# Kernel optimization log

Hardware: AMD Instinct MI355X
Metric: run time of the kernel (lower is better)

Reference implementation:

```python
import jax, jax.numpy as jnp
import numpy as np

BLANK = 0
BEAM = 5


def setup_inputs() -> dict:
    key = jax.random.key(0)
    ks = jax.random.split(key, 8)
    B, T, H, V = 8, 128, 1024, 4096
    s = lambda k, sh, sc: jax.random.normal(k, sh, dtype=jnp.float32) * sc
    return {
        "tn_output": s(ks[0], (B, T, H), 1.0),
        "E": s(ks[1], (V, H), 0.02),
        "W_ih": s(ks[2], (4 * H, H), 0.02),
        "W_hh": s(ks[3], (4 * H, H), 0.02),
        "b_lstm": jnp.zeros((4 * H,), jnp.float32),
        "W_tn": s(ks[4], (H, H), 0.02),
        "W_pn": s(ks[5], (H, H), 0.02),
        "b_joint": jnp.zeros((H,), jnp.float32),
        "W_out": s(ks[6], (H, V), 0.02),
        "b_out": jnp.zeros((V,), jnp.float32),
    }


def _beam_search(tn_output, E, W_ih, W_hh, b_lstm, W_tn, W_pn, b_joint, W_out, b_out):
    # Batched RNN-T beam search (one expansion per frame, all B*K hyps batched).
    B, T, H = tn_output.shape
    V = E.shape[0]
    K = BEAM
    NEG = jnp.float32(-1e9)

    tn_proj = jnp.einsum('bth,hd->btd', tn_output, W_tn)  # [B,T,H] precomputed

    tokens0 = jnp.full((B, K), BLANK, jnp.int32)          # last emitted token
    h0 = jnp.zeros((B, K, H), tn_output.dtype)
    c0 = jnp.zeros((B, K, H), tn_output.dtype)
    scores0 = jnp.full((B, K), NEG).at[:, 0].set(0.0)     # only beam 0 alive
    preds0 = jnp.zeros((B, K, T), jnp.int32)
    lens0 = jnp.zeros((B, K), jnp.int32)

    def step(carry, tn_t):  # tn_t: [B,H] (projected TN output at frame t)
        tokens, h, c, scores, preds, lens = carry
        # --- prediction network (LSTM cell) over all B*K hyps at once ---
        emb = E[tokens]                                   # [B,K,H]
        gates = emb @ W_ih.T + h @ W_hh.T + b_lstm        # [B,K,4H]
        i_g, f_g, g_g, o_g = jnp.split(gates, 4, axis=-1)
        c_new = jax.nn.sigmoid(f_g) * c + jax.nn.sigmoid(i_g) * jnp.tanh(g_g)
        h_new = jax.nn.sigmoid(o_g) * jnp.tanh(c_new)     # [B,K,H]
        # --- joint network ---
        joint = jnp.tanh(tn_t[:, None, :] + h_new @ W_pn + b_joint)
        logp = jax.nn.log_softmax(joint @ W_out + b_out, axis=-1)  # [B,K,V]
        # --- beam expand + prune ---
        cand = (scores[:, :, None] + logp).reshape(B, K * V)
        top_s, top_i = jax.lax.top_k(cand, K)             # [B,K]
        parent = top_i // V
        tok = (top_i % V).astype(jnp.int32)
        is_blank = tok == BLANK

        g2 = lambda x: jnp.take_along_axis(x, parent, axis=1)
        g3 = lambda x: jnp.take_along_axis(x, parent[:, :, None], axis=1)
        # blank keeps the parent's pre-step decoder state; non-blank advances it
        h_next = jnp.where(is_blank[:, :, None], g3(h), g3(h_new))
        c_next = jnp.where(is_blank[:, :, None], g3(c), g3(c_new))
        tokens_next = jnp.where(is_blank, g2(tokens), tok)
        lens_p = g2(lens)
        preds_p = g3(preds.reshape(B, K, -1)).reshape(B, K, preds.shape[-1])
        pos = (jnp.arange(preds.shape[-1])[None, None, :] == lens_p[:, :, None]) & (~is_blank)[:, :, None]
        preds_next = jnp.where(pos, tok[:, :, None], preds_p)
        lens_next = lens_p + (~is_blank).astype(jnp.int32)
        return (tokens_next, h_next, c_next, top_s, preds_next, lens_next), None

    carry, _ = jax.lax.scan(step, (tokens0, h0, c0, scores0, preds0, lens0),
                            jnp.swapaxes(tn_proj, 0, 1))
    _, _, _, scores, preds, lens = carry
    # original normalizes by len(prediction) which includes the leading blank -> lens+1
    norm = scores / (lens.astype(scores.dtype) + 1.0)
    return preds, lens, norm


def reference(tn_output, E, W_ih, W_hh, b_lstm, W_tn, W_pn, b_joint, W_out, b_out):
    preds, lens, norm = _beam_search(tn_output, E, W_ih, W_hh, b_lstm,
                                     W_tn, W_pn, b_joint, W_out, b_out)
    best = jnp.argmax(norm, axis=1)                       # [B]
    best_preds = jnp.take_along_axis(preds, best[:, None, None], axis=1)[:, 0]  # [B,T]
    best_lens = jnp.take_along_axis(lens, best[:, None], axis=1)[:, 0]          # [B]
    mean_score = jnp.exp(jnp.max(norm, axis=1)).mean()
    return best_preds, best_lens, mean_score, norm
```

## Files before the change

### kernel.cpp

```cpp
#include <hip/hip_runtime.h>
#include <math.h>

#define HH 1024
#define VV 4096
#define TSTEPS 128
#define NB 256
#define NT 512

typedef float  floatx4 __attribute__((ext_vector_type(4)));
typedef int    intx4   __attribute__((ext_vector_type(4)));


__device__ __forceinline__ float sigf(float x) { return 1.0f / (1.0f + expf(-x)); }

__device__ __forceinline__ float rowsum16(float x) {
  x += __int_as_float(__builtin_amdgcn_update_dpp(0, __float_as_int(x), 0x111, 0xf, 0xf, true));
  x += __int_as_float(__builtin_amdgcn_update_dpp(0, __float_as_int(x), 0x112, 0xf, 0xf, true));
  x += __int_as_float(__builtin_amdgcn_update_dpp(0, __float_as_int(x), 0x114, 0xf, 0xf, true));
  x += __int_as_float(__builtin_amdgcn_update_dpp(0, __float_as_int(x), 0x118, 0xf, 0xf, true));
  return x;
}

__device__ __forceinline__ void ins5(float* bv, int* bi, float v, int i) {
#pragma unroll
  for (int j = 0; j < 5; ++j) {
    if (v > bv[j] || (v == bv[j] && i < bi[j])) {
#pragma unroll
      for (int s = 4; s > j; --s) { bv[s] = bv[s - 1]; bi[s] = bi[s - 1]; }
      bv[j] = v; bi[j] = i;
      break;
    }
  }
}


__device__ __forceinline__ float ldcc(const float* p) {
  float v;
  asm volatile("global_load_dword %0, %1, off sc0 sc1\n\ts_waitcnt vmcnt(0)"
               : "=&v"(v) : "v"(p) : "memory");
  return v;
}
__device__ __forceinline__ int ldcci(const int* p) {
  int v;
  asm volatile("global_load_dword %0, %1, off sc0 sc1\n\ts_waitcnt vmcnt(0)"
               : "=&v"(v) : "v"(p) : "memory");
  return v;
}
__device__ __forceinline__ floatx4 ldcc4(const float* p) {
  floatx4 v;
  asm volatile("global_load_dwordx4 %0, %1, off sc0 sc1\n\ts_waitcnt vmcnt(0)"
               : "=&v"(v) : "v"(p) : "memory");
  return v;
}
__device__ __forceinline__ void stcc(float* p, float v) {
  asm volatile("global_store_dword %0, %1, off sc0 sc1" :: "v"(p), "v"(v) : "memory");
}
__device__ __forceinline__ void stcci(int* p, int v) {
  asm volatile("global_store_dword %0, %1, off sc0 sc1" :: "v"(p), "v"(v) : "memory");
}
__device__ __forceinline__ void stcc4(float* p, floatx4 v) {
  asm volatile("global_store_dwordx4 %0, %1, off sc0 sc1" :: "v"(p), "v"(v) : "memory");
}
__device__ __forceinline__ void stcc4i(int* p, intx4 v) {
  asm volatile("global_store_dwordx4 %0, %1, off sc0 sc1" :: "v"(p), "v"(v) : "memory");
}

__device__ __forceinline__ void ldwt(floatx4& v, const float* p) {
  asm volatile("global_load_dwordx4 %0, %1, off\n\ts_waitcnt vmcnt(0)"
               : "=&v"(v) : "v"(p));
}

__device__ __forceinline__ void ldcc4x5(const float* p0, const float* p1, const float* p2,
                                        const float* p3, const float* p4,
                                        floatx4& v0, floatx4& v1, floatx4& v2,
                                        floatx4& v3, floatx4& v4) {
  asm volatile(
      "global_load_dwordx4 %0, %5, off sc0 sc1\n\t"
      "global_load_dwordx4 %1, %6, off sc0 sc1\n\t"
      "global_load_dwordx4 %2, %7, off sc0 sc1\n\t"
      "global_load_dwordx4 %3, %8, off sc0 sc1\n\t"
      "global_load_dwordx4 %4, %9, off sc0 sc1\n\t"
      "s_waitcnt vmcnt(0)"
      : "=&v"(v0), "=&v"(v1), "=&v"(v2), "=&v"(v3), "=&v"(v4)
      : "v"(p0), "v"(p1), "v"(p2), "v"(p3), "v"(p4)
      : "memory");
}

__device__ __forceinline__ void ldcc_top5(const float* pv, const int* pi,
                                          float tv[5], int ti[5]) {
  floatx4 a; float a1; intx4 b; int b1;
  asm volatile(
      "global_load_dwordx4 %0, %4, off sc0 sc1\n\t"
      "global_load_dword   %1, %5, off sc0 sc1\n\t"
      "global_load_dwordx4 %2, %6, off sc0 sc1\n\t"
      "global_load_dword   %3, %7, off sc0 sc1\n\t"
      "s_waitcnt vmcnt(0)"
      : "=&v"(a), "=&v"(a1), "=&v"(b), "=&v"(b1)
      : "v"(pv), "v"(pv + 4), "v"(pi), "v"(pi + 4)
      : "memory");
  tv[0] = a.x; tv[1] = a.y; tv[2] = a.z; tv[3] = a.w; tv[4] = a1;
  ti[0] = b.x; ti[1] = b.y; ti[2] = b.z; ti[3] = b.w; ti[4] = b1;
}

__device__ __forceinline__ void ldcc_state(const float* ps, const int* pl, const int* pt,
                                           const int* pp, const int* pb,
                                           float& sc, int& ln, int& tk, int& pr, int& bl) {
  asm volatile(
      "global_load_dword %0, %5, off sc0 sc1\n\t"
      "global_load_dword %1, %6, off sc0 sc1\n\t"
      "global_load_dword %2, %7, off sc0 sc1\n\t"
      "global_load_dword %3, %8, off sc0 sc1\n\t"
      "global_load_dword %4, %9, off sc0 sc1\n\t"
      "s_waitcnt vmcnt(0)"
      : "=&v"(sc), "=&v"(ln), "=&v"(tk), "=&v"(pr), "=&v"(bl)
      : "v"(ps), "v"(pl), "v"(pt), "v"(pp), "v"(pb)
      : "memory");
}


__global__ __launch_bounds__(256) void k_transp(const float* __restrict__ in,
                                                float* __restrict__ out, int R, int C) {
  __shared__ float tile[32][33];
  int c0 = blockIdx.x * 32, r0 = blockIdx.y * 32;
  int tx = threadIdx.x & 31, ty = threadIdx.x >> 5;
#pragma unroll
  for (int i = 0; i < 32; i += 8) tile[ty + i][tx] = in[(long)(r0 + ty + i) * C + c0 + tx];
  __syncthreads();
#pragma unroll
  for (int i = 0; i < 32; i += 8) out[(long)(c0 + ty + i) * R + r0 + tx] = tile[tx][ty + i];
}

__global__ __launch_bounds__(256) void k_tnproj(const float* __restrict__ A,
                                                const float* __restrict__ B,
                                                float* __restrict__ C) {
  __shared__ float As[64][20];
  __shared__ float Bs[16][68];
  int tid = threadIdx.x, blk = blockIdx.x;
  int bx = blk & 15, by = blk >> 4;
  int tx = tid & 15, ty = tid >> 4;
  float acc[4][4];
#pragma unroll
  for (int i = 0; i < 4; i++)
#pragma unroll
    for (int j = 0; j < 4; j++) acc[i][j] = 0.f;
  for (int k0 = 0; k0 < 1024; k0 += 16) {
    {
      int row = tid >> 2, q = tid & 3;
      float4 v = *(const float4*)&A[(long)(by * 64 + row) * 1024 + k0 + q * 4];
      As[row][q * 4] = v.x; As[row][q * 4 + 1] = v.y; As[row][q * 4 + 2] = v.z; As[row][q * 4 + 3] = v.w;
    }
    {
      int row = tid >> 4, q = tid & 15;
      float4 v = *(const float4*)&B[(long)(k0 + row) * 1024 + bx * 64 + q * 4];
      *(float4*)&Bs[row][q * 4] = v;
    }
    __syncthreads();
#pragma unroll
    for (int kk = 0; kk < 16; kk++) {
      float a0 = As[ty * 4][kk], a1 = As[ty * 4 + 1][kk], a2 = As[ty * 4 + 2][kk], a3 = As[ty * 4 + 3][kk];
      float4 b4 = *(const float4*)&Bs[kk][tx * 4];
      acc[0][0] += a0 * b4.x; acc[0][1] += a0 * b4.y; acc[0][2] += a0 * b4.z; acc[0][3] += a0 * b4.w;
      acc[1][0] += a1 * b4.x; acc[1][1] += a1 * b4.y; acc[1][2] += a1 * b4.z; acc[1][3] += a1 * b4.w;
      acc[2][0] += a2 * b4.x; acc[2][1] += a2 * b4.y; acc[2][2] += a2 * b4.z; acc[2][3] += a2 * b4.w;
      acc[3][0] += a3 * b4.x; acc[3][1] += a3 * b4.y; acc[3][2] += a3 * b4.z; acc[3][3] += a3 * b4.w;
    }
    __syncthreads();
  }
#pragma unroll
  for (int i = 0; i < 4; i++) {
    float4 v = make_float4(acc[i][0], acc[i][1], acc[i][2], acc[i][3]);
    *(float4*)&C[(long)(by * 64 + ty * 4 + i) * 1024 + bx * 64 + tx * 4] = v;
  }
}


__global__ __launch_bounds__(NT, 1) void k_beam(
    const float* __restrict__ E, const float* __restrict__ Wih,
    const float* __restrict__ Whh, const float* __restrict__ b_lstm,
    const float* __restrict__ tn_proj, const float* __restrict__ WpnT,
    const float* __restrict__ b_joint, const float* __restrict__ WoutT,
    const float* __restrict__ b_out,
    float* __restrict__ h_pre0, float* __restrict__ h_pre1,
    float* __restrict__ c_pre0, float* __restrict__ c_pre1,
    float* __restrict__ h_new0, float* __restrict__ h_new1,
    float* __restrict__ c_new0, float* __restrict__ c_new1,
    float* __restrict__ joint, float* __restrict__ expsum_part,
    float* __restrict__ top5v, int* __restrict__ top5i,
    int* __restrict__ preds0, int* __restrict__ preds1,
    float* __restrict__ gscores, int* __restrict__ glens,
    int* __restrict__ gtokens, int* __restrict__ gpar, int* __restrict__ gblank,
    unsigned int* bar, float* __restrict__ out) {
  int tid = threadIdx.x, blk = blockIdx.x;
  int wav = tid >> 6, lane = tid & 63;

  __shared__ float xs[10240];
  __shared__ float part[640];
  __shared__ float s_scores[40], s_scls[5];
  __shared__ int s_tokens[40], s_lens[40], s_par[40], s_blank[40];
  __shared__ float s_csel[160];
  __shared__ float wtv[40];
  __shared__ int wti[40];
  __shared__ int s_best[8];
  __shared__ float s_maxn[8];
  float4* xs4 = (float4*)xs;

  floatx4 wihr[2][4], whhr[2][4], wpnr[4], woutr[2][4];
#pragma unroll
  for (int rr = 0; rr < 2; ++rr) {
    int gr = wav * 2 + rr;
    int jg = blk * 4 + (gr >> 2), g = gr & 3;
#pragma unroll
    for (int c = 0; c < 4; ++c) {
      ldwt(wihr[rr][c], &Wih[(long)(g * HH + jg) * HH + c * 256 + lane * 4]);
      ldwt(whhr[rr][c], &Whh[(long)(g * HH + jg) * HH + c * 256 + lane * 4]);
    }
  }
  {
    int d = blk * 4 + (wav >> 1);
#pragma unroll
    for (int c = 0; c < 4; ++c)
      ldwt(wpnr[c], &WpnT[(long)d * HH + c * 256 + lane * 4]);
  }
#pragma unroll
  for (int r = 0; r < 2; ++r) {
    int v = blk * 16 + wav * 2 + r;
#pragma unroll
    for (int c = 0; c < 4; ++c)
      ldwt(woutr[r][c], &WoutT[(long)v * HH + c * 256 + lane * 4]);
  }

  if (tid < 40) {
    s_scores[tid] = ((tid % 5) == 0) ? 0.f : -1e9f;
    s_tokens[tid] = 0; s_lens[tid] = 0; s_par[tid] = tid; s_blank[tid] = 1;
  }
  __syncthreads();

  unsigned int round = 0;
  auto gsync = [&]() {
    asm volatile("s_waitcnt vmcnt(0)" ::: "memory");
    __syncthreads();
    if (tid == 0)
      __hip_atomic_fetch_add(&bar[(blk & 15) * 16], 1u, __ATOMIC_RELAXED, __HIP_MEMORY_SCOPE_AGENT);
    ++round;
    if (tid < 16) {
      unsigned int tgt = round * 16u;
      while (__hip_atomic_load(&bar[tid * 16], __ATOMIC_RELAXED, __HIP_MEMORY_SCOPE_AGENT) < tgt)
        __builtin_amdgcn_s_sleep(2);
    }
    __syncthreads();
  };

  auto preds_update = [&](int u) {
    const int* pip = ((u - 1) & 1) ? preds1 : preds0;
    int* pop = (u & 1) ? preds1 : preds0;
    int m0 = blk * 10;
    for (int cell = tid; cell < 1280; cell += NT) {
      int j = cell >> 7, pos = cell & 127, gj = m0 + j;
      int isb = s_blank[gj];
      int plen = s_lens[gj] - (isb ? 0 : 1);
      int v = ldcci(&pip[s_par[gj] * 128 + pos]);
      if (!isb && pos == plen) v = s_tokens[gj];
      stcci(&pop[gj * 128 + pos], v);
    }
  };

  for (int t = 0; t < TSTEPS; ++t) {
    const float* h_pre_in = (t & 1) ? h_pre1 : h_pre0;
    const float* h_new_in = (t & 1) ? h_new1 : h_new0;
    const float* c_pre_in = (t & 1) ? c_pre1 : c_pre0;
    const float* c_new_in = (t & 1) ? c_new1 : c_new0;
    float* h_pre_o = (t & 1) ? h_pre0 : h_pre1;
    float* h_new_o = (t & 1) ? h_new0 : h_new1;
    float* c_pre_o = (t & 1) ? c_pre0 : c_pre1;
    float* c_new_o = (t & 1) ? c_new0 : c_new1;

    if (t > 0) {
      if (tid < 40) {
        float sc; int ln, tk, pr, bl;
        ldcc_state(&gscores[tid], &glens[tid], &gtokens[tid], &gpar[tid], &gblank[tid],
                   sc, ln, tk, pr, bl);
        s_scores[tid] = sc; s_lens[tid] = ln; s_tokens[tid] = tk;
        s_par[tid] = pr; s_blank[tid] = bl;
      }
      __syncthreads();
      if (tid < 160) {
        int mg = tid >> 2, j = tid & 3;
        const float* cb = s_blank[mg] ? c_pre_in : c_new_in;
        s_csel[tid] = ldcc(&cb[(long)s_par[mg] * HH + blk * 4 + j]);
      }
      if (blk < 4) preds_update(t);
    }

    {
      int mat = tid >> 8, k4f = (tid & 255) * 4;
      for (int cc = 0; cc < 8; ++cc) {
        int ch = (blk + cc) & 7;
        int mbase = ch * 5;
        if (mat == 0) {
#pragma unroll
          for (int i = 0; i < 5; ++i)
            xs4[i * 512 + tid] = *(const float4*)&E[(long)s_tokens[mbase + i] * HH + k4f];
        } else if (t == 0) {
          floatx4 z = {0.f, 0.f, 0.f, 0.f};
#pragma unroll
          for (int i = 0; i < 5; ++i) {
            *(floatx4*)(xs4 + i * 512 + tid) = z;
            if (blk == ch) stcc4(&h_pre_o[(long)(mbase + i) * HH + k4f], z);
          }
        } else {
          const float* p[5];
#pragma unroll
          for (int i = 0; i < 5; ++i) {
            int mg = mbase + i;
            const float* hb = s_blank[mg] ? h_pre_in : h_new_in;
            p[i] = &hb[(long)s_par[mg] * HH + k4f];
          }
          floatx4 v0, v1, v2, v3, v4;
          ldcc4x5(p[0], p[1], p[2], p[3], p[4], v0, v1, v2, v3, v4);
          *(floatx4*)(xs4 + 0 * 512 + tid) = v0;
          *(floatx4*)(xs4 + 1 * 512 + tid) = v1;
          *(floatx4*)(xs4 + 2 * 512 + tid) = v2;
          *(floatx4*)(xs4 + 3 * 512 + tid) = v3;
          *(floatx4*)(xs4 + 4 * 512 + tid) = v4;
          if (blk == ch) {
            stcc4(&h_pre_o[(long)(mbase + 0) * HH + k4f], v0);
            stcc4(&h_pre_o[(long)(mbase + 1) * HH + k4f], v1);
            stcc4(&h_pre_o[(long)(mbase + 2) * HH + k4f], v2);
            stcc4(&h_pre_o[(long)(mbase + 3) * HH + k4f], v3);
            stcc4(&h_pre_o[(long)(mbase + 4) * HH + k4f], v4);
          }
        }
        __syncthreads();
        float acc[5][2];
#pragma unroll
        for (int m = 0; m < 5; ++m) { acc[m][0] = 0.f; acc[m][1] = 0.f; }
#pragma unroll
        for (int m = 0; m < 5; ++m) {
#pragma unroll
          for (int c = 0; c < 4; ++c) {
            float4 x = xs4[m * 512 + c * 64 + lane];
#pragma unroll
            for (int rr = 0; rr < 2; ++rr) {
              floatx4 ww = wihr[rr][c];
              acc[m][rr] += x.x * ww.x; acc[m][rr] += x.y * ww.y;
              acc[m][rr] += x.z * ww.z; acc[m][rr] += x.w * ww.w;
            }
          }
#pragma unroll
          for (int c = 0; c < 4; ++c) {
            float4 x = xs4[m * 512 + 256 + c * 64 + lane];
#pragma unroll
            for (int rr = 0; rr < 2; ++rr) {
              floatx4 ww = whhr[rr][c];
              acc[m][rr] += x.x * ww.x; acc[m][rr] += x.y * ww.y;
              acc[m][rr] += x.z * ww.z; acc[m][rr] += x.w * ww.w;
            }
          }
        }
#pragma unroll
        for (int m = 0; m < 5; ++m) {
          acc[m][0] = rowsum16(acc[m][0]);
          acc[m][1] = rowsum16(acc[m][1]);
        }
        if ((lane & 15) == 15) {
          int grp = lane >> 4;
#pragma unroll
          for (int m = 0; m < 5; ++m) {
            part[(wav * 4 + grp) * 10 + m * 2] = acc[m][0];
            part[(wav * 4 + grp) * 10 + m * 2 + 1] = acc[m][1];
          }
        }
        __syncthreads();
        if (tid < 20) {
          int mloc = tid >> 2, j = tid & 3;
          int mg = mbase + mloc, jglob = blk * 4 + j;
          float gi = 0.f, gf = 0.f, gg = 0.f, go = 0.f;
#pragma unroll
          for (int r = 0; r < 4; ++r) {
            gi += part[((j * 2) * 4 + r) * 10 + mloc * 2];
            gf += part[((j * 2) * 4 + r) * 10 + mloc * 2 + 1];
            gg += part[((j * 2 + 1) * 4 + r) * 10 + mloc * 2];
            go += part[((j * 2 + 1) * 4 + r) * 10 + mloc * 2 + 1];
          }
          gi += b_lstm[jglob]; gf += b_lstm[HH + jglob];
          gg += b_lstm[2 * HH + jglob]; go += b_lstm[3 * HH + jglob];
          float csel = (t == 0) ? 0.f : s_csel[mg * 4 + j];
          float cn = sigf(gf) * csel + sigf(gi) * tanhf(gg);
          float hn = sigf(go) * tanhf(cn);
          long o = (long)mg * HH + jglob;
          stcc(&h_new_o[o], hn); stcc(&c_new_o[o], cn); stcc(&c_pre_o[o], csel);
        }
      }
    }
    gsync();

    {
      int mrow = tid >> 8, k4f = (tid & 255) * 4;
      for (int cc = 0; cc < 4; ++cc) {
        int ch = (blk + cc) & 3;
        int mbase = ch * 10;
        floatx4 v0, v1, v2, v3, v4;
        ldcc4x5(&h_new_o[(long)(mbase + mrow + 0) * HH + k4f],
                &h_new_o[(long)(mbase + mrow + 2) * HH + k4f],
                &h_new_o[(long)(mbase + mrow + 4) * HH + k4f],
                &h_new_o[(long)(mbase + mrow + 6) * HH + k4f],
                &h_new_o[(long)(mbase + mrow + 8) * HH + k4f],
                v0, v1, v2, v3, v4);
        *(floatx4*)(xs4 + 0 * 512 + tid) = v0;
        *(floatx4*)(xs4 + 1 * 512 + tid) = v1;
        *(floatx4*)(xs4 + 2 * 512 + tid) = v2;
        *(floatx4*)(xs4 + 3 * 512 + tid) = v3;
        *(floatx4*)(xs4 + 4 * 512 + tid) = v4;
        __syncthreads();
        float accj[5];
#pragma unroll
        for (int m = 0; m < 5; ++m) accj[m] = 0.f;
        int mh = (wav & 1) * 5;
#pragma unroll
        for (int m = 0; m < 5; ++m) {
#pragma unroll
          for (int c = 0; c < 4; ++c) {
            float4 x = xs4[(mh + m) * 256 + c * 64 + lane];
            floatx4 ww = wpnr[c];
            accj[m] += x.x * ww.x; accj[m] += x.y * ww.y;
            accj[m] += x.z * ww.z; accj[m] += x.w * ww.w;
          }
        }
#pragma unroll
        for (int m = 0; m < 5; ++m) accj[m] = rowsum16(accj[m]);
        if ((lane & 15) == 15) {
          int grp = lane >> 4;
#pragma unroll
          for (int m = 0; m < 5; ++m) part[(wav * 4 + grp) * 5 + m] = accj[m];
        }
        __syncthreads();
        if (tid < 40) {
          int mloc = tid >> 2, d = tid & 3;
          int wv = d * 2 + (mloc >= 5 ? 1 : 0), m5 = mloc % 5;
          float s = 0.f;
#pragma unroll
          for (int r = 0; r < 4; ++r) s += part[(wv * 4 + r) * 5 + m5];
          int mg = mbase + mloc, dglob = blk * 4 + d, b = mg / 5;
          stcc(&joint[(long)mg * HH + dglob],
               tanhf(s + tn_proj[((long)b * TSTEPS + t) * HH + dglob] + b_joint[dglob]));
        }
      }
    }
    gsync();

    {
      int mrow = tid >> 8, k4f = (tid & 255) * 4;
      for (int cc = 0; cc < 4; ++cc) {
        int ch = (blk + cc) & 3;
        int mbase = ch * 10;
        floatx4 v0, v1, v2, v3, v4;
        ldcc4x5(&joint[(long)(mbase + mrow + 0) * HH + k4f],
                &joint[(long)(mbase + mrow + 2) * HH + k4f],
                &joint[(long)(mbase + mrow + 4) * HH + k4f],
                &joint[(long)(mbase + mrow + 6) * HH + k4f],
                &joint[(long)(mbase + mrow + 8) * HH + k4f],
                v0, v1, v2, v3, v4);
        *(floatx4*)(xs4 + 0 * 512 + tid) = v0;
        *(floatx4*)(xs4 + 1 * 512 + tid) = v1;
        *(floatx4*)(xs4 + 2 * 512 + tid) = v2;
        *(floatx4*)(xs4 + 3 * 512 + tid) = v3;
        *(floatx4*)(xs4 + 4 * 512 + tid) = v4;
        __syncthreads();
        float accl[10][2];
#pragma unroll
        for (int m = 0; m < 10; ++m) { accl[m][0] = 0.f; accl[m][1] = 0.f; }
#pragma unroll
        for (int m = 0; m < 10; ++m)
#pragma unroll
          for (int c = 0; c < 4; ++c) {
            float4 x = xs4[m * 256 + c * 64 + lane];
#pragma unroll
            for (int r = 0; r < 2; ++r) {
              floatx4 ww = woutr[r][c];
              accl[m][r] += x.x * ww.x; accl[m][r] += x.y * ww.y;
              accl[m][r] += x.z * ww.z; accl[m][r] += x.w * ww.w;
            }
          }
#pragma unroll
        for (int m = 0; m < 10; ++m) {
          accl[m][0] = rowsum16(accl[m][0]);
          accl[m][1] = rowsum16(accl[m][1]);
        }
        if ((lane & 15) == 15) {
          int grp = lane >> 4;
#pragma unroll
          for (int m = 0; m < 10; ++m) {
            part[(wav * 4 + grp) * 20 + m * 2] = accl[m][0];
            part[(wav * 4 + grp) * 20 + m * 2 + 1] = accl[m][1];
          }
        }
        __syncthreads();
        if (tid < 160) {
          int mloc = tid >> 4, vloc = tid & 15;
          int wv = vloc >> 1, rowr = vloc & 1;
          float s = 0.f;
#pragma unroll
          for (int r = 0; r < 4; ++r) s += part[(wv * 4 + r) * 20 + mloc * 2 + rowr];
          int v = blk * 16 + vloc, mg = mbase + mloc;
          float lg = s + b_out[v];
          float e = rowsum16(expf(lg));
          if ((tid & 15) == 15) stcc(&expsum_part[mg * 256 + blk], e);
          float cv = lg; int ci = (mg % 5) * 4096 + v;
          float tv[5]; int ti5[5];
#pragma unroll
          for (int r5 = 0; r5 < 5; ++r5) {
            float mv = cv; int mi = ci;
#pragma unroll
            for (int off2 = 1; off2 < 16; off2 <<= 1) {
              float ov = __shfl_xor(mv, off2, 16);
              int oi = __shfl_xor(mi, off2, 16);
              if (ov > mv || (ov == mv && oi < mi)) { mv = ov; mi = oi; }
            }
            if (cv == mv && ci == mi) cv = -3.0e38f;
            tv[r5] = mv; ti5[r5] = mi;
          }
          if ((tid & 15) == 0) {
            int toff = (mg * 256 + blk) * 8;
            floatx4 tvv = {tv[0], tv[1], tv[2], tv[3]};
            intx4 tiv = {ti5[0], ti5[1], ti5[2], ti5[3]};
            stcc4(&top5v[toff], tvv); stcc(&top5v[toff + 4], tv[4]);
            stcc4i(&top5i[toff], tiv); stcci(&top5i[toff + 4], ti5[4]);
          }
        }
      }
    }
    gsync();

    if (blk < 8) {
      int b = blk;
      if (wav < 5) {
        int kp = wav;
        const float* ep = &expsum_part[(b * 5 + kp) * 256];
        floatx4 e4 = ldcc4(&ep[lane * 4]);
        float tl = ((e4.x + e4.y) + e4.z) + e4.w;
        part[kp * 64 + lane] = tl;
        if (lane == 0) {
          float ssum = 0.f;
          for (int i = 0; i < 64; ++i) ssum += part[kp * 64 + i];
          s_scls[kp] = s_scores[b * 5 + kp] - logf(ssum);
        }
      }
      __syncthreads();
      float bv[5]; int bi5[5];
#pragma unroll
      for (int q = 0; q < 5; ++q) { bv[q] = -3.0e38f; bi5[q] = 0x7fffffff; }
      for (int e = wav * 160 + lane; e < wav * 160 + 160; e += 64) {
        int kp = e >> 8, blkc = e & 255;
        float base = s_scls[kp];
        int off = ((b * 5 + kp) * 256 + blkc) * 8;
        float tv[5]; int ti5[5];
        ldcc_top5(&top5v[off], &top5i[off], tv, ti5);
#pragma unroll
        for (int q = 0; q < 5; ++q) ins5(bv, bi5, tv[q] + base, ti5[q]);
      }
      float myv = 0.f; int myi = 0;
#pragma unroll
      for (int r = 0; r < 5; ++r) {
        float mv = bv[0]; int mi = bi5[0];
#pragma unroll
        for (int off2 = 1; off2 < 64; off2 <<= 1) {
          float ov = __shfl_xor(mv, off2, 64);
          int oi = __shfl_xor(mi, off2, 64);
          if (ov > mv || (ov == mv && oi < mi)) { mv = ov; mi = oi; }
        }
        if (bv[0] == mv && bi5[0] == mi) {
          bv[0] = bv[1]; bi5[0] = bi5[1]; bv[1] = bv[2]; bi5[1] = bi5[2];
          bv[2] = bv[3]; bi5[2] = bi5[3]; bv[3] = bv[4]; bi5[3] = bi5[4];
          bv[4] = -3.0e38f; bi5[4] = 0x7fffffff;
        }
        if (lane == r) { myv = mv; myi = mi; }
      }
      if (lane < 5) { wtv[wav * 5 + lane] = myv; wti[wav * 5 + lane] = myi; }
      __syncthreads();
      if (wav == 0) {
        float cv = (lane < 40) ? wtv[lane] : -3.0e38f;
        int ci = (lane < 40) ? wti[lane] : 0x7fffffff;
#pragma unroll
        for (int r = 0; r < 5; ++r) {
          float mv = cv; int mi = ci;
#pragma unroll
          for (int off2 = 1; off2 < 64; off2 <<= 1) {
            float ov = __shfl_xor(mv, off2, 64);
            int oi = __shfl_xor(mi, off2, 64);
            if (ov > mv || (ov == mv && oi < mi)) { mv = ov; mi = oi; }
          }
          if (cv == mv && ci == mi) cv = -3.0e38f;
          if (lane == r) { myv = mv; myi = mi; }
        }
        if (lane < 5) {
          int kp = myi >> 12, tok = myi & 4095;
          int isb = (tok == 0) ? 1 : 0;
          int pg = b * 5 + kp, slot = b * 5 + lane;
          stcc(&gscores[slot], myv); stcci(&gpar[slot], pg); stcci(&gblank[slot], isb);
          stcci(&gtokens[slot], isb ? s_tokens[pg] : tok);
          stcci(&glens[slot], s_lens[pg] + (isb ? 0 : 1));
        }
      }
    }
    gsync();
  }

  if (tid < 40) {
    float sc; int ln, tk, pr, bl;
    ldcc_state(&gscores[tid], &glens[tid], &gtokens[tid], &gpar[tid], &gblank[tid],
               sc, ln, tk, pr, bl);
    s_scores[tid] = sc; s_lens[tid] = ln; s_tokens[tid] = tk;
    s_par[tid] = pr; s_blank[tid] = bl;
  }
  __syncthreads();
  if (blk < 4) preds_update(TSTEPS);
  gsync();

  if (blk == 0) {
    if (tid < 40) out[1033 + tid] = s_scores[tid] / (float)(s_lens[tid] + 1);
    if (tid < 8) {
      float bvn = -3.0e38f; int bk = 0;
      for (int k = 0; k < 5; ++k) {
        float n = s_scores[tid * 5 + k] / (float)(s_lens[tid * 5 + k] + 1);
        if (n > bvn) { bvn = n; bk = k; }
      }
      s_best[tid] = bk; s_maxn[tid] = bvn;
      out[1024 + tid] = (float)s_lens[tid * 5 + bk];
    }
    __syncthreads();
    if (tid == 0) {
      float s = 0.f;
      for (int b = 0; b < 8; ++b) s += expf(s_maxn[b]);
      out[1032] = s / 8.f;
    }
    for (int cI = tid; cI < 1024; cI += NT) {
      int b = cI >> 7, pos = cI & 127;
      out[cI] = (float)ldcci(&preds0[(b * 5 + s_best[b]) * 128 + pos]);
    }
  }
}


extern "C" void kernel_launch(void* const* d_in, const int* in_sizes, int n_in,
                              void* d_out, int out_size, void* d_ws, size_t ws_size,
                              hipStream_t stream) {
  const float* tn   = (const float*)d_in[0];
  const float* E    = (const float*)d_in[1];
  const float* Wih  = (const float*)d_in[2];
  const float* Whh  = (const float*)d_in[3];
  const float* bl   = (const float*)d_in[4];
  const float* Wtn  = (const float*)d_in[5];
  const float* Wpn  = (const float*)d_in[6];
  const float* bj   = (const float*)d_in[7];
  const float* Wout = (const float*)d_in[8];
  const float* bo   = (const float*)d_in[9];
  float* out = (float*)d_out;

  unsigned int* bar = (unsigned int*)d_ws;
  float* w = (float*)d_ws + 256;
  size_t off = 0;
  float* tn_proj = w + off; off += 1048576;
  float* WpnT    = w + off; off += 1048576;
  float* WoutT   = w + off; off += 4194304;
  float* joint   = w + off; off += 40960;
  float* expsum  = w + off; off += 10240;
  float* top5v   = w + off; off += 81920;
  float* h_pre0  = w + off; off += 40960;
  float* h_pre1  = w + off; off += 40960;
  float* c_pre0  = w + off; off += 40960;
  float* c_pre1  = w + off; off += 40960;
  float* h_new0  = w + off; off += 40960;
  float* h_new1  = w + off; off += 40960;
  float* c_new0  = w + off; off += 40960;
  float* c_new1  = w + off; off += 40960;
  float* gscores = w + off; off += 40;
  int* ib = (int*)(w + off);
  int* top5i   = ib; ib += 81920;
  int* preds0  = ib; ib += 5120;
  int* preds1  = ib; ib += 5120;
  int* glens   = ib; ib += 40;
  int* gtokens = ib; ib += 40;
  int* gpar    = ib; ib += 40;
  int* gblank  = ib; ib += 40;
  if (ws_size < (size_t)(256 + off + 92320) * 4) return;

  hipMemsetAsync(bar, 0, 1024, stream);
  hipMemsetAsync(preds0, 0, 5120 * sizeof(int), stream);
  k_transp<<<dim3(32, 32), 256, 0, stream>>>(Wpn, WpnT, 1024, 1024);
  k_transp<<<dim3(128, 32), 256, 0, stream>>>(Wout, WoutT, 1024, 4096);
  k_tnproj<<<256, 256, 0, stream>>>(tn, Wtn, tn_proj);

  void* args[] = { (void*)&E, (void*)&Wih, (void*)&Whh, (void*)&bl,
                   (void*)&tn_proj, (void*)&WpnT, (void*)&bj, (void*)&WoutT, (void*)&bo,
                   (void*)&h_pre0, (void*)&h_pre1, (void*)&c_pre0, (void*)&c_pre1,
                   (void*)&h_new0, (void*)&h_new1, (void*)&c_new0, (void*)&c_new1,
                   (void*)&joint, (void*)&expsum, (void*)&top5v, (void*)&top5i,
                   (void*)&preds0, (void*)&preds1, (void*)&gscores, (void*)&glens,
                   (void*)&gtokens, (void*)&gpar, (void*)&gblank,
                   (void*)&bar, (void*)&out };
  hipLaunchCooperativeKernel((void*)k_beam, dim3(NB), dim3(NT), args, 0, stream);
}
```

Before: 12.54 ms.

## Triple-buffer activation loads via async global-to-LDS with prefetch in each phase

Replaces the synchronous register-staged loads of embeddings, hidden states, and joint activations with global_load_lds direct-to-LDS transfers into a three-slot LDS ring. Each phase prefetches up to three chunks ahead and uses counted vmcnt waits, so memory latency overlaps with the dot-product compute of earlier chunks. The preds copy is also unrolled so that all of its loads are issued together before a single wait. This triples the LDS footprint, which may reduce occupancy. It also relies on hand-tuned waitcnt counts and cache-coherence bits for data written by other blocks in the persistent kernel.

```diff
diff --git a/kernel.cpp b/kernel.cpp
--- a/kernel.cpp
+++ b/kernel.cpp
@@ -9,6 +9,10 @@
 
 typedef float  floatx4 __attribute__((ext_vector_type(4)));
 typedef int    intx4   __attribute__((ext_vector_type(4)));
+
+#define GLL(gp, lp, aux) __builtin_amdgcn_global_load_lds( \
+    (const __attribute__((address_space(1))) unsigned int*)(gp), \
+    (__attribute__((address_space(3))) unsigned int*)(lp), 16, 0, aux)
 
 
 __device__ __forceinline__ float sigf(float x) { return 1.0f / (1.0f + expf(-x)); }
@@ -68,22 +72,6 @@
 __device__ __forceinline__ void ldwt(floatx4& v, const float* p) {
   asm volatile("global_load_dwordx4 %0, %1, off\n\ts_waitcnt vmcnt(0)"
                : "=&v"(v) : "v"(p));
-}
-
-__device__ __forceinline__ void ldcc4x5(const float* p0, const float* p1, const float* p2,
-                                        const float* p3, const float* p4,
-                                        floatx4& v0, floatx4& v1, floatx4& v2,
-                                        floatx4& v3, floatx4& v4) {
-  asm volatile(
-      "global_load_dwordx4 %0, %5, off sc0 sc1\n\t"
-      "global_load_dwordx4 %1, %6, off sc0 sc1\n\t"
-      "global_load_dwordx4 %2, %7, off sc0 sc1\n\t"
-      "global_load_dwordx4 %3, %8, off sc0 sc1\n\t"
-      "global_load_dwordx4 %4, %9, off sc0 sc1\n\t"
-      "s_waitcnt vmcnt(0)"
-      : "=&v"(v0), "=&v"(v1), "=&v"(v2), "=&v"(v3), "=&v"(v4)
-      : "v"(p0), "v"(p1), "v"(p2), "v"(p3), "v"(p4)
-      : "memory");
 }
 
 __device__ __forceinline__ void ldcc_top5(const float* pv, const int* pi,
@@ -193,7 +181,7 @@
   int tid = threadIdx.x, blk = blockIdx.x;
   int wav = tid >> 6, lane = tid & 63;
 
-  __shared__ float xs[10240];
+  __shared__ float xs[3 * 10240];
   __shared__ float part[640];
   __shared__ float s_scores[40], s_scls[5];
   __shared__ int s_tokens[40], s_lens[40], s_par[40], s_blank[40];
@@ -202,7 +190,6 @@
   __shared__ int wti[40];
   __shared__ int s_best[8];
   __shared__ float s_maxn[8];
-  float4* xs4 = (float4*)xs;
 
   floatx4 wihr[2][4], whhr[2][4], wpnr[4], woutr[2][4];
 #pragma unroll
@@ -264,6 +251,8 @@
     }
   };
 
+  int mat = tid >> 8, k4f = (tid & 255) * 4;
+
   for (int t = 0; t < TSTEPS; ++t) {
     const float* h_pre_in = (t & 1) ? h_pre1 : h_pre0;
     const float* h_new_in = (t & 1) ? h_new1 : h_new0;
@@ -288,49 +277,92 @@
         const float* cb = s_blank[mg] ? c_pre_in : c_new_in;
         s_csel[tid] = ldcc(&cb[(long)s_par[mg] * HH + blk * 4 + j]);
       }
-      if (blk < 4) preds_update(t);
+      if (blk < 4) {
+        const int* pip = ((t - 1) & 1) ? preds1 : preds0;
+        int* pop = (t & 1) ? preds1 : preds0;
+        int m0b = blk * 10;
+        int jA = tid >> 7, pA = tid & 127, gA = m0b + jA;
+        int cB = tid + 512, jB = cB >> 7, pB = cB & 127, gB = m0b + jB;
+        int cC = tid + 1024, jC = cC >> 7, pC = cC & 127, gC = m0b + jC;
+        const int* aA = &pip[s_par[gA] * 128 + pA];
+        const int* aB = &pip[s_par[gB] * 128 + pB];
+        int vA, vB, vC = 0;
+        if (tid < 256) {
+          const int* aC = &pip[s_par[gC] * 128 + pC];
+          asm volatile(
+              "global_load_dword %0, %3, off sc0 sc1\n\t"
+              "global_load_dword %1, %4, off sc0 sc1\n\t"
+              "global_load_dword %2, %5, off sc0 sc1\n\t"
+              "s_waitcnt vmcnt(0)"
+              : "=&v"(vA), "=&v"(vB), "=&v"(vC)
+              : "v"(aA), "v"(aB), "v"(aC) : "memory");
+        } else {
+          asm volatile(
+              "global_load_dword %0, %2, off sc0 sc1\n\t"
+              "global_load_dword %1, %3, off sc0 sc1\n\t"
+              "s_waitcnt vmcnt(0)"
+              : "=&v"(vA), "=&v"(vB)
+              : "v"(aA), "v"(aB) : "memory");
+        }
+        {
+          int isb = s_blank[gA], plen = s_lens[gA] - (isb ? 0 : 1);
+          if (!isb && pA == plen) vA = s_tokens[gA];
+          stcci(&pop[gA * 128 + pA], vA);
+        }
+        {
+          int isb = s_blank[gB], plen = s_lens[gB] - (isb ? 0 : 1);
+          if (!isb && pB == plen) vB = s_tokens[gB];
+          stcci(&pop[gB * 128 + pB], vB);
+        }
+        if (tid < 256) {
+          int isb = s_blank[gC], plen = s_lens[gC] - (isb ? 0 : 1);
+          if (!isb && pC == plen) vC = s_tokens[gC];
+          stcci(&pop[gC * 128 + pC], vC);
+        }
+      }
     }
 
     {
-      int mat = tid >> 8, k4f = (tid & 255) * 4;
+      auto g_issue = [&](int cc) {
+        int ch = (blk + cc) & 7, mbase = ch * 5;
+        float* dst = xs + (cc % 3) * 10240;
+        if (mat == 0) {
+#pragma unroll
+          for (int i = 0; i < 5; ++i)
+            GLL(&E[(long)s_tokens[mbase + i] * HH + k4f], dst + i * 2048 + tid * 4, 0);
+        } else if (t > 0) {
+#pragma unroll
+          for (int i = 0; i < 5; ++i) {
+            int mg = mbase + i;
+            const float* hb = s_blank[mg] ? h_pre_in : h_new_in;
+            GLL(&hb[(long)s_par[mg] * HH + k4f], dst + i * 2048 + tid * 4, 17);
+          }
+        }
+        __builtin_amdgcn_sched_barrier(0);
+      };
+      g_issue(0); g_issue(1); g_issue(2);
       for (int cc = 0; cc < 8; ++cc) {
         int ch = (blk + cc) & 7;
         int mbase = ch * 5;
-        if (mat == 0) {
+        float4* xb = (float4*)(xs + (cc % 3) * 10240);
+        if (cc < 6)      asm volatile("s_waitcnt vmcnt(10)" ::: "memory");
+        else if (cc == 6) asm volatile("s_waitcnt vmcnt(5)" ::: "memory");
+        else             asm volatile("s_waitcnt vmcnt(0)" ::: "memory");
+        __builtin_amdgcn_sched_barrier(0);
+        if (t == 0 && mat == 1) {
+          floatx4 z = {0.f, 0.f, 0.f, 0.f};
+#pragma unroll
+          for (int i = 0; i < 5; ++i) {
+            *(floatx4*)(xb + i * 512 + tid) = z;
+            if (blk == ch) stcc4(&h_pre_o[(long)(mbase + i) * HH + k4f], z);
+          }
+        }
+        __syncthreads();
+        if (t > 0 && mat == 1 && blk == ch) {
 #pragma unroll
           for (int i = 0; i < 5; ++i)
-            xs4[i * 512 + tid] = *(const float4*)&E[(long)s_tokens[mbase + i] * HH + k4f];
-        } else if (t == 0) {
-          floatx4 z = {0.f, 0.f, 0.f, 0.f};
-#pragma unroll
-          for (int i = 0; i < 5; ++i) {
-            *(floatx4*)(xs4 + i * 512 + tid) = z;
-            if (blk == ch) stcc4(&h_pre_o[(long)(mbase + i) * HH + k4f], z);
-          }
-        } else {
-          const float* p[5];
-#pragma unroll
-          for (int i = 0; i < 5; ++i) {
-            int mg = mbase + i;
-            const float* hb = s_blank[mg] ? h_pre_in : h_new_in;
-            p[i] = &hb[(long)s_par[mg] * HH + k4f];
-          }
-          floatx4 v0, v1, v2, v3, v4;
-          ldcc4x5(p[0], p[1], p[2], p[3], p[4], v0, v1, v2, v3, v4);
-          *(floatx4*)(xs4 + 0 * 512 + tid) = v0;
-          *(floatx4*)(xs4 + 1 * 512 + tid) = v1;
-          *(floatx4*)(xs4 + 2 * 512 + tid) = v2;
-          *(floatx4*)(xs4 + 3 * 512 + tid) = v3;
-          *(floatx4*)(xs4 + 4 * 512 + tid) = v4;
-          if (blk == ch) {
-            stcc4(&h_pre_o[(long)(mbase + 0) * HH + k4f], v0);
-            stcc4(&h_pre_o[(long)(mbase + 1) * HH + k4f], v1);
-            stcc4(&h_pre_o[(long)(mbase + 2) * HH + k4f], v2);
-            stcc4(&h_pre_o[(long)(mbase + 3) * HH + k4f], v3);
-            stcc4(&h_pre_o[(long)(mbase + 4) * HH + k4f], v4);
-          }
-        }
-        __syncthreads();
+            stcc4(&h_pre_o[(long)(mbase + i) * HH + k4f], *(floatx4*)(xb + i * 512 + tid));
+        }
         float acc[5][2];
 #pragma unroll
         for (int m = 0; m < 5; ++m) { acc[m][0] = 0.f; acc[m][1] = 0.f; }
@@ -338,7 +370,7 @@
         for (int m = 0; m < 5; ++m) {
 #pragma unroll
           for (int c = 0; c < 4; ++c) {
-            float4 x = xs4[m * 512 + c * 64 + lane];
+            float4 x = xb[m * 512 + c * 64 + lane];
 #pragma unroll
             for (int rr = 0; rr < 2; ++rr) {
               floatx4 ww = wihr[rr][c];
@@ -348,7 +380,7 @@
           }
 #pragma unroll
           for (int c = 0; c < 4; ++c) {
-            float4 x = xs4[m * 512 + 256 + c * 64 + lane];
+            float4 x = xb[m * 512 + 256 + c * 64 + lane];
 #pragma unroll
             for (int rr = 0; rr < 2; ++rr) {
               floatx4 ww = whhr[rr][c];
@@ -390,27 +422,29 @@
           long o = (long)mg * HH + jglob;
           stcc(&h_new_o[o], hn); stcc(&c_new_o[o], cn); stcc(&c_pre_o[o], csel);
         }
+        if (cc < 5) g_issue(cc + 3);
       }
     }
     gsync();
 
     {
-      int mrow = tid >> 8, k4f = (tid & 255) * 4;
+      auto j_issue = [&](int cc) {
+        int ch = (blk + cc) & 3, mbase = ch * 10;
+        float* dst = xs + (cc % 3) * 10240;
+#pragma unroll
+        for (int i = 0; i < 5; ++i)
+          GLL(&h_new_o[(long)(mbase + mat + 2 * i) * HH + k4f], dst + i * 2048 + tid * 4, 17);
+        __builtin_amdgcn_sched_barrier(0);
+      };
+      j_issue(0); j_issue(1); j_issue(2);
       for (int cc = 0; cc < 4; ++cc) {
         int ch = (blk + cc) & 3;
         int mbase = ch * 10;
-        floatx4 v0, v1, v2, v3, v4;
-        ldcc4x5(&h_new_o[(long)(mbase + mrow + 0) * HH + k4f],
-                &h_new_o[(long)(mbase + mrow + 2) * HH + k4f],
-                &h_new_o[(long)(mbase + mrow + 4) * HH + k4f],
-                &h_new_o[(long)(mbase + mrow + 6) * HH + k4f],
-                &h_new_o[(long)(mbase + mrow + 8) * HH + k4f],
-                v0, v1, v2, v3, v4);
-        *(floatx4*)(xs4 + 0 * 512 + tid) = v0;
-        *(floatx4*)(xs4 + 1 * 512 + tid) = v1;
-        *(floatx4*)(xs4 + 2 * 512 + tid) = v2;
-        *(floatx4*)(xs4 + 3 * 512 + tid) = v3;
-        *(floatx4*)(xs4 + 4 * 512 + tid) = v4;
+        float4* xb = (float4*)(xs + (cc % 3) * 10240);
+        if (cc < 2)      asm volatile("s_waitcnt vmcnt(10)" ::: "memory");
+        else if (cc == 2) asm volatile("s_waitcnt vmcnt(5)" ::: "memory");
+        else             asm volatile("s_waitcnt vmcnt(0)" ::: "memory");
+        __builtin_amdgcn_sched_barrier(0);
         __syncthreads();
         float accj[5];
 #pragma unroll
@@ -420,7 +454,7 @@
         for (int m = 0; m < 5; ++m) {
 #pragma unroll
           for (int c = 0; c < 4; ++c) {
-            float4 x = xs4[(mh + m) * 256 + c * 64 + lane];
+            float4 x = xb[(mh + m) * 256 + c * 64 + lane];
             floatx4 ww = wpnr[c];
             accj[m] += x.x * ww.x; accj[m] += x.y * ww.y;
             accj[m] += x.z * ww.z; accj[m] += x.w * ww.w;
@@ -444,27 +478,29 @@
           stcc(&joint[(long)mg * HH + dglob],
                tanhf(s + tn_proj[((long)b * TSTEPS + t) * HH + dglob] + b_joint[dglob]));
         }
+        if (cc < 1) j_issue(cc + 3);
       }
     }
     gsync();
 
     {
-      int mrow = tid >> 8, k4f = (tid & 255) * 4;
+      auto l_issue = [&](int cc) {
+        int ch = (blk + cc) & 3, mbase = ch * 10;
+        float* dst = xs + (cc % 3) * 10240;
+#pragma unroll
+        for (int i = 0; i < 5; ++i)
+          GLL(&joint[(long)(mbase + mat + 2 * i) * HH + k4f], dst + i * 2048 + tid * 4, 17);
+        __builtin_amdgcn_sched_barrier(0);
+      };
+      l_issue(0); l_issue(1); l_issue(2);
       for (int cc = 0; cc < 4; ++cc) {
         int ch = (blk + cc) & 3;
         int mbase = ch * 10;
-        floatx4 v0, v1, v2, v3, v4;
-        ldcc4x5(&joint[(long)(mbase + mrow + 0) * HH + k4f],
-                &joint[(long)(mbase + mrow + 2) * HH + k4f],
-                &joint[(long)(mbase + mrow + 4) * HH + k4f],
-                &joint[(long)(mbase + mrow + 6) * HH + k4f],
-                &joint[(long)(mbase + mrow + 8) * HH + k4f],
-                v0, v1, v2, v3, v4);
-        *(floatx4*)(xs4 + 0 * 512 + tid) = v0;
-        *(floatx4*)(xs4 + 1 * 512 + tid) = v1;
-        *(floatx4*)(xs4 + 2 * 512 + tid) = v2;
-        *(floatx4*)(xs4 + 3 * 512 + tid) = v3;
-        *(floatx4*)(xs4 + 4 * 512 + tid) = v4;
+        float4* xb = (float4*)(xs + (cc % 3) * 10240);
+        if (cc < 2)      asm volatile("s_waitcnt vmcnt(10)" ::: "memory");
+        else if (cc == 2) asm volatile("s_waitcnt vmcnt(5)" ::: "memory");
+        else             asm volatile("s_waitcnt vmcnt(0)" ::: "memory");
+        __builtin_amdgcn_sched_barrier(0);
         __syncthreads();
         float accl[10][2];
 #pragma unroll
@@ -473,7 +509,7 @@
         for (int m = 0; m < 10; ++m)
 #pragma unroll
           for (int c = 0; c < 4; ++c) {
-            float4 x = xs4[m * 256 + c * 64 + lane];
+            float4 x = xb[m * 256 + c * 64 + lane];
 #pragma unroll
             for (int r = 0; r < 2; ++r) {
               floatx4 ww = woutr[r][c];
@@ -527,6 +563,7 @@
             stcc4i(&top5i[toff], tiv); stcci(&top5i[toff + 4], ti5[4]);
           }
         }
+        if (cc < 1) l_issue(cc + 3);
       }
     }
     gsync();
```

Measured after the change: 14.65 ms. +16.8%, slower.

## Stage broadcast activations into per-XCD L2-local buffers with XCD-level barriers

Applied to the files above, without the earlier changes.

Each XCD (read via HW_REG_XCC_ID) now gets a private copy of the gathered h/c state, h_new and joint rows. The blocks on that XCD fill the copy cooperatively using coherent loads, then synchronize with a per-XCD barrier. The repeated broadcast reads then use sc0-only loads that can hit the local L2, instead of system-coherent loads that bypass cache on every block. The cost is an extra copy pass, three extra XCD-level barriers per timestep, more workspace, and reliance on L2 coherence within an XCD.

```diff
diff --git a/kernel.cpp b/kernel.cpp
--- a/kernel.cpp
+++ b/kernel.cpp
@@ -8,6 +8,7 @@
 #define NT 512
 
 typedef float  floatx4 __attribute__((ext_vector_type(4)));
+typedef float  floatx2 __attribute__((ext_vector_type(2)));
 typedef int    intx4   __attribute__((ext_vector_type(4)));
 
 
@@ -65,25 +66,46 @@
   asm volatile("global_store_dwordx4 %0, %1, off sc0 sc1" :: "v"(p), "v"(v) : "memory");
 }
 
-__device__ __forceinline__ void ldwt(floatx4& v, const float* p) {
-  asm volatile("global_load_dwordx4 %0, %1, off\n\ts_waitcnt vmcnt(0)"
-               : "=&v"(v) : "v"(p));
-}
-
-__device__ __forceinline__ void ldcc4x5(const float* p0, const float* p1, const float* p2,
-                                        const float* p3, const float* p4,
-                                        floatx4& v0, floatx4& v1, floatx4& v2,
-                                        floatx4& v3, floatx4& v4) {
+__device__ __forceinline__ float ldl2(const float* p) {
+  float v;
+  asm volatile("global_load_dword %0, %1, off sc0\n\ts_waitcnt vmcnt(0)"
+               : "=&v"(v) : "v"(p) : "memory");
+  return v;
+}
+__device__ __forceinline__ void ldl2x5(const float* p0, const float* p1, const float* p2,
+                                       const float* p3, const float* p4,
+                                       floatx4& v0, floatx4& v1, floatx4& v2,
+                                       floatx4& v3, floatx4& v4) {
   asm volatile(
-      "global_load_dwordx4 %0, %5, off sc0 sc1\n\t"
-      "global_load_dwordx4 %1, %6, off sc0 sc1\n\t"
-      "global_load_dwordx4 %2, %7, off sc0 sc1\n\t"
-      "global_load_dwordx4 %3, %8, off sc0 sc1\n\t"
-      "global_load_dwordx4 %4, %9, off sc0 sc1\n\t"
+      "global_load_dwordx4 %0, %5, off sc0\n\t"
+      "global_load_dwordx4 %1, %6, off sc0\n\t"
+      "global_load_dwordx4 %2, %7, off sc0\n\t"
+      "global_load_dwordx4 %3, %8, off sc0\n\t"
+      "global_load_dwordx4 %4, %9, off sc0\n\t"
       "s_waitcnt vmcnt(0)"
       : "=&v"(v0), "=&v"(v1), "=&v"(v2), "=&v"(v3), "=&v"(v4)
       : "v"(p0), "v"(p1), "v"(p2), "v"(p3), "v"(p4)
       : "memory");
+}
+
+__device__ __forceinline__ void ldcc2x2(const float* p0, const float* p1,
+                                        floatx2& a, floatx2& b) {
+  asm volatile(
+      "global_load_dwordx2 %0, %2, off sc0 sc1\n\t"
+      "global_load_dwordx2 %1, %3, off sc0 sc1\n\t"
+      "s_waitcnt vmcnt(0)"
+      : "=&v"(a), "=&v"(b) : "v"(p0), "v"(p1) : "memory");
+}
+__device__ __forceinline__ floatx2 ldcc2(const float* p) {
+  floatx2 v;
+  asm volatile("global_load_dwordx2 %0, %1, off sc0 sc1\n\ts_waitcnt vmcnt(0)"
+               : "=&v"(v) : "v"(p) : "memory");
+  return v;
+}
+
+__device__ __forceinline__ void ldwt(floatx4& v, const float* p) {
+  asm volatile("global_load_dwordx4 %0, %1, off\n\ts_waitcnt vmcnt(0)"
+               : "=&v"(v) : "v"(p));
 }
 
 __device__ __forceinline__ void ldcc_top5(const float* pv, const int* pi,
@@ -189,6 +211,7 @@
     int* __restrict__ preds0, int* __restrict__ preds1,
     float* __restrict__ gscores, int* __restrict__ glens,
     int* __restrict__ gtokens, int* __restrict__ gpar, int* __restrict__ gblank,
+    float* __restrict__ xcdbufA, float* __restrict__ xcdbufB,
     unsigned int* bar, float* __restrict__ out) {
   int tid = threadIdx.x, blk = blockIdx.x;
   int wav = tid >> 6, lane = tid & 63;
@@ -202,7 +225,14 @@
   __shared__ int wti[40];
   __shared__ int s_best[8];
   __shared__ float s_maxn[8];
+  __shared__ int s_xrank, s_xn;
   float4* xs4 = (float4*)xs;
+
+  int xcd;
+  asm("s_getreg_b32 %0, hwreg(HW_REG_XCC_ID)" : "=s"(xcd));
+  xcd &= 7;
+  float* xcdA = xcdbufA + (long)xcd * 40960;
+  float* xcdB = xcdbufB + (long)xcd * 40960;
 
   floatx4 wihr[2][4], whhr[2][4], wpnr[4], woutr[2][4];
 #pragma unroll
@@ -233,6 +263,9 @@
     s_scores[tid] = ((tid % 5) == 0) ? 0.f : -1e9f;
     s_tokens[tid] = 0; s_lens[tid] = 0; s_par[tid] = tid; s_blank[tid] = 1;
   }
+  if (tid == 0)
+    s_xrank = (int)__hip_atomic_fetch_add(&bar[256 + xcd], 1u,
+                                          __ATOMIC_RELAXED, __HIP_MEMORY_SCOPE_AGENT);
   __syncthreads();
 
   unsigned int round = 0;
@@ -250,6 +283,27 @@
     __syncthreads();
   };
 
+  unsigned int xround = 0;
+  auto xsync = [&]() {
+    asm volatile("s_waitcnt vmcnt(0)" ::: "memory");
+    __syncthreads();
+    if (tid == 0)
+      __hip_atomic_fetch_add(&bar[320 + xcd * 16], 1u, __ATOMIC_RELAXED, __HIP_MEMORY_SCOPE_AGENT);
+    ++xround;
+    if (tid == 0) {
+      unsigned int tgt = xround * (unsigned int)s_xn;
+      while (__hip_atomic_load(&bar[320 + xcd * 16], __ATOMIC_RELAXED, __HIP_MEMORY_SCOPE_AGENT) < tgt)
+        __builtin_amdgcn_s_sleep(2);
+    }
+    __syncthreads();
+  };
+
+  gsync();
+  if (tid == 0)
+    s_xn = (int)__hip_atomic_load(&bar[256 + xcd], __ATOMIC_RELAXED, __HIP_MEMORY_SCOPE_AGENT);
+  __syncthreads();
+  int xrank = s_xrank, xn = s_xn;
+
   auto preds_update = [&](int u) {
     const int* pip = ((u - 1) & 1) ? preds1 : preds0;
     int* pop = (u & 1) ? preds1 : preds0;
@@ -264,6 +318,9 @@
     }
   };
 
+  int mat = tid >> 8, k4f = (tid & 255) * 4;
+  int seg = tid * 2;
+
   for (int t = 0; t < TSTEPS; ++t) {
     const float* h_pre_in = (t & 1) ? h_pre1 : h_pre0;
     const float* h_new_in = (t & 1) ? h_new1 : h_new0;
@@ -283,16 +340,24 @@
         s_par[tid] = pr; s_blank[tid] = bl;
       }
       __syncthreads();
+      for (int row = xrank; row < 40; row += xn) {
+        const float* hb = s_blank[row] ? h_pre_in : h_new_in;
+        const float* cb = s_blank[row] ? c_pre_in : c_new_in;
+        long so = (long)s_par[row] * HH + seg;
+        floatx2 hv, cv2;
+        ldcc2x2(&hb[so], &cb[so], hv, cv2);
+        *(floatx2*)&xcdA[row * HH + seg] = hv;
+        *(floatx2*)&xcdB[row * HH + seg] = cv2;
+      }
+      if (blk < 4) preds_update(t);
+      xsync();
       if (tid < 160) {
         int mg = tid >> 2, j = tid & 3;
-        const float* cb = s_blank[mg] ? c_pre_in : c_new_in;
-        s_csel[tid] = ldcc(&cb[(long)s_par[mg] * HH + blk * 4 + j]);
-      }
-      if (blk < 4) preds_update(t);
+        s_csel[tid] = ldl2(&xcdB[mg * HH + blk * 4 + j]);
+      }
     }
 
     {
-      int mat = tid >> 8, k4f = (tid & 255) * 4;
       for (int cc = 0; cc < 8; ++cc) {
         int ch = (blk + cc) & 7;
         int mbase = ch * 5;
@@ -308,15 +373,10 @@
             if (blk == ch) stcc4(&h_pre_o[(long)(mbase + i) * HH + k4f], z);
           }
         } else {
-          const float* p[5];
-#pragma unroll
-          for (int i = 0; i < 5; ++i) {
-            int mg = mbase + i;
-            const float* hb = s_blank[mg] ? h_pre_in : h_new_in;
-            p[i] = &hb[(long)s_par[mg] * HH + k4f];
-          }
           floatx4 v0, v1, v2, v3, v4;
-          ldcc4x5(p[0], p[1], p[2], p[3], p[4], v0, v1, v2, v3, v4);
+          ldl2x5(&xcdA[(mbase + 0) * HH + k4f], &xcdA[(mbase + 1) * HH + k4f],
+                 &xcdA[(mbase + 2) * HH + k4f], &xcdA[(mbase + 3) * HH + k4f],
+                 &xcdA[(mbase + 4) * HH + k4f], v0, v1, v2, v3, v4);
           *(floatx4*)(xs4 + 0 * 512 + tid) = v0;
           *(floatx4*)(xs4 + 1 * 512 + tid) = v1;
           *(floatx4*)(xs4 + 2 * 512 + tid) = v2;
@@ -395,17 +455,22 @@
     gsync();
 
     {
-      int mrow = tid >> 8, k4f = (tid & 255) * 4;
+      for (int row = xrank; row < 40; row += xn) {
+        floatx2 v = ldcc2(&h_new_o[(long)row * HH + seg]);
+        *(floatx2*)&xcdA[row * HH + seg] = v;
+      }
+      xsync();
+      int mrow = mat;
       for (int cc = 0; cc < 4; ++cc) {
         int ch = (blk + cc) & 3;
         int mbase = ch * 10;
         floatx4 v0, v1, v2, v3, v4;
-        ldcc4x5(&h_new_o[(long)(mbase + mrow + 0) * HH + k4f],
-                &h_new_o[(long)(mbase + mrow + 2) * HH + k4f],
-                &h_new_o[(long)(mbase + mrow + 4) * HH + k4f],
-                &h_new_o[(long)(mbase + mrow + 6) * HH + k4f],
-                &h_new_o[(long)(mbase + mrow + 8) * HH + k4f],
-                v0, v1, v2, v3, v4);
+        ldl2x5(&xcdA[(mbase + mrow + 0) * HH + k4f],
+               &xcdA[(mbase + mrow + 2) * HH + k4f],
+               &xcdA[(mbase + mrow + 4) * HH + k4f],
+               &xcdA[(mbase + mrow + 6) * HH + k4f],
+               &xcdA[(mbase + mrow + 8) * HH + k4f],
+               v0, v1, v2, v3, v4);
         *(floatx4*)(xs4 + 0 * 512 + tid) = v0;
         *(floatx4*)(xs4 + 1 * 512 + tid) = v1;
         *(floatx4*)(xs4 + 2 * 512 + tid) = v2;
@@ -449,17 +514,22 @@
     gsync();
 
     {
-      int mrow = tid >> 8, k4f = (tid & 255) * 4;
+      for (int row = xrank; row < 40; row += xn) {
+        floatx2 v = ldcc2(&joint[(long)row * HH + seg]);
+        *(floatx2*)&xcdA[row * HH + seg] = v;
+      }
+      xsync();
+      int mrow = mat;
       for (int cc = 0; cc < 4; ++cc) {
         int ch = (blk + cc) & 3;
         int mbase = ch * 10;
         floatx4 v0, v1, v2, v3, v4;
-        ldcc4x5(&joint[(long)(mbase + mrow + 0) * HH + k4f],
-                &joint[(long)(mbase + mrow + 2) * HH + k4f],
-                &joint[(long)(mbase + mrow + 4) * HH + k4f],
-                &joint[(long)(mbase + mrow + 6) * HH + k4f],
-                &joint[(long)(mbase + mrow + 8) * HH + k4f],
-                v0, v1, v2, v3, v4);
+        ldl2x5(&xcdA[(mbase + mrow + 0) * HH + k4f],
+               &xcdA[(mbase + mrow + 2) * HH + k4f],
+               &xcdA[(mbase + mrow + 4) * HH + k4f],
+               &xcdA[(mbase + mrow + 6) * HH + k4f],
+               &xcdA[(mbase + mrow + 8) * HH + k4f],
+               v0, v1, v2, v3, v4);
         *(floatx4*)(xs4 + 0 * 512 + tid) = v0;
         *(floatx4*)(xs4 + 1 * 512 + tid) = v1;
         *(floatx4*)(xs4 + 2 * 512 + tid) = v2;
@@ -657,7 +727,7 @@
   float* out = (float*)d_out;
 
   unsigned int* bar = (unsigned int*)d_ws;
-  float* w = (float*)d_ws + 256;
+  float* w = (float*)d_ws + 512;
   size_t off = 0;
   float* tn_proj = w + off; off += 1048576;
   float* WpnT    = w + off; off += 1048576;
@@ -673,6 +743,8 @@
   float* h_new1  = w + off; off += 40960;
   float* c_new0  = w + off; off += 40960;
   float* c_new1  = w + off; off += 40960;
+  float* xcdA    = w + off; off += 327680;
+  float* xcdB    = w + off; off += 327680;
   float* gscores = w + off; off += 40;
   int* ib = (int*)(w + off);
   int* top5i   = ib; ib += 81920;
@@ -682,9 +754,9 @@
   int* gtokens = ib; ib += 40;
   int* gpar    = ib; ib += 40;
   int* gblank  = ib; ib += 40;
-  if (ws_size < (size_t)(256 + off + 92320) * 4) return;
-
-  hipMemsetAsync(bar, 0, 1024, stream);
+  if (ws_size < (size_t)(512 + off + 92320) * 4) return;
+
+  hipMemsetAsync(bar, 0, 2048, stream);
   hipMemsetAsync(preds0, 0, 5120 * sizeof(int), stream);
   k_transp<<<dim3(32, 32), 256, 0, stream>>>(Wpn, WpnT, 1024, 1024);
   k_transp<<<dim3(128, 32), 256, 0, stream>>>(Wout, WoutT, 1024, 4096);
@@ -697,6 +769,7 @@
                    (void*)&joint, (void*)&expsum, (void*)&top5v, (void*)&top5i,
                    (void*)&preds0, (void*)&preds1, (void*)&gscores, (void*)&glens,
                    (void*)&gtokens, (void*)&gpar, (void*)&gblank,
+                   (void*)&xcdA, (void*)&xcdB,
                    (void*)&bar, (void*)&out };
   hipLaunchCooperativeKernel((void*)k_beam, dim3(NB), dim3(NT), args, 0, stream);
 }
```

New measurement: 14.42 ms. 15.0% more time.
